# Kernel tuning notes

Hardware: AMD Instinct MI355X
Metric: run time of the kernel (lower is better)

## Reference

```python
import jax, jax.numpy as jnp
import numpy as np

L = 2      # layer_num
H = 64     # hid_dim == in_dim (required by final .view(B, N, F))


def setup_inputs() -> dict:
    key = jax.random.key(0)
    k = jax.random.split(key, 5)
    B, T, N, Fd = 64, 48, 256, H
    s = 1.0 / np.sqrt(H)  # PyTorch GRUCell init scale
    return {
        "x": jax.random.normal(k[0], (B, T, N, Fd), dtype=jnp.float32),
        "Wih": jax.random.uniform(k[1], (L, 3 * H, H), minval=-s, maxval=s, dtype=jnp.float32),
        "Whh": jax.random.uniform(k[2], (L, 3 * H, H), minval=-s, maxval=s, dtype=jnp.float32),
        "bih": jax.random.uniform(k[3], (L, 3 * H), minval=-s, maxval=s, dtype=jnp.float32),
        "bhh": jax.random.uniform(k[4], (L, 3 * H), minval=-s, maxval=s, dtype=jnp.float32),
    }


def _ngru_forward(x, Wih, Whh, bih, bhh):
    B, T, N, Fd = x.shape
    # (T, B*N, F): time-major sequence; each layer sees the SAME input x_t
    # (layers are parallel, not stacked, per the original module).
    xs = x.transpose(1, 0, 2, 3).reshape(T, B * N, Fd)
    h0 = jnp.zeros((L, B * N, H), dtype=x.dtype)

    def step(h, x_t):
        # gi: (L, B*N, 3H), gh: (L, B*N, 3H)
        gi = jnp.einsum('bf,lgf->lbg', x_t, Wih) + bih[:, None, :]
        gh = jnp.einsum('lbh,lgh->lbg', h, Whh) + bhh[:, None, :]
        gi_r, gi_z, gi_n = jnp.split(gi, 3, axis=-1)
        gh_r, gh_z, gh_n = jnp.split(gh, 3, axis=-1)
        r = jax.nn.sigmoid(gi_r + gh_r)
        z = jax.nn.sigmoid(gi_z + gh_z)
        n = jnp.tanh(gi_n + r * gh_n)
        h_new = (1.0 - z) * n + z * h
        return h_new, None

    h_final, _ = jax.lax.scan(step, h0, xs)
    # out = h of LAST layer, viewed back as (B, N, F) (requires H == Fd)
    return h_final[-1].reshape(B, N, H)


def reference(x, Wih, Whh, bih, bhh):
    return _ngru_forward(x, Wih, Whh, bih, bhh)
```

## Files before the change

### kernel.cpp

```cpp
#include <hip/hip_runtime.h>
#include <math.h>


#define TT 48
#define HH 64
#define GG 192
#define NN 256
#define RPB 32
#define NTHREADS 512
#define AK 136
#define HBUF (RPB*AK)

typedef _Float16 h8 __attribute__((ext_vector_type(8)));
typedef __attribute__((ext_vector_type(4))) float f32x4;
typedef __attribute__((ext_vector_type(2))) unsigned u32x2;

__device__ __forceinline__ float sigm(float v) {
    return __builtin_amdgcn_rcpf(1.f + __expf(-v));
}
__device__ __forceinline__ float tanh_f(float v) {
    float a = fabsf(v);
    float e = __expf(2.f * a);
    float t = 1.f - 2.f * __builtin_amdgcn_rcpf(e + 1.f);
    return v < 0.f ? -t : t;
}
__device__ __forceinline__ unsigned pkh2(float a, float b) {
    union { _Float16 h[2]; unsigned u; } c;
    c.h[0] = (_Float16)a; c.h[1] = (_Float16)b;
    return c.u;
}

#define MF(A, B, C) __builtin_amdgcn_mfma_f32_16x16x32_f16(A, B, C, 0, 0, 0)

__global__ __launch_bounds__(NTHREADS)
__attribute__((amdgpu_waves_per_eu(4, 4)))
void ngru_mfma12(const float* __restrict__ x,
                 const float* __restrict__ Wih,
                 const float* __restrict__ Whh,
                 const float* __restrict__ bih,
                 const float* __restrict__ bhh,
                 float* __restrict__ out)
{
    extern __shared__ __align__(16) _Float16 lds_h[];

    const int tid  = threadIdx.x;
    const int lane = tid & 63;
    const int wv   = tid >> 6;
    const int m    = wv >> 2;
    const int nw   = wv & 3;
    const int c0   = lane & 15;
    const int rq   = lane >> 4;
    const int j    = nw * 16 + c0;

    const int grow0 = blockIdx.x * RPB;
    const int bb    = grow0 / NN;
    const int n0    = grow0 % NN;

    const float* Wi = Wih + GG * HH;
    const float* Wh = Whh + GG * HH;

    h8 Bf[12];
    #pragma unroll
    for (int g = 0; g < 4; ++g) {
        const int ktlo = (g == 3) ? 2 : 0;
        const int kthi = (g == 2) ? 2 : 4;
        #pragma unroll
        for (int kt = ktlo; kt < kthi; ++kt) {
            const int slot = (g < 2) ? g * 4 + kt : 8 + (g - 2) * 2 + (kt & 1);
            const bool isWi = (kt < 2);
            const int gbase = (g >= 2) ? 2 : g;
            const float* src = (isWi ? Wi : Wh)
                             + (gbase * 64 + j) * HH + (kt & 1) * 32 + rq * 8;
            h8 f;
            #pragma unroll
            for (int q = 0; q < 8; ++q) f[q] = (_Float16)src[q];
            Bf[slot] = f;
        }
    }

    const float brz  = bih[GG + j]      + bhh[GG + j];
    const float bzz  = bih[GG + 64 + j] + bhh[GG + 64 + j];
    const float bin_ = bih[GG + 128 + j];
    const float bhn_ = bhh[GG + 128 + j];

    const int xrow = tid >> 4;
    const int xc   = (tid & 15) * 4;
    {
        *(u32x2*)(lds_h + xrow * AK + 64 + xc) = (u32x2){0u, 0u};
        const float* xsrc = x + ((size_t)(bb * TT) * NN + n0 + xrow) * HH + xc;
        float4 p = *(const float4*)xsrc;
        *(u32x2*)(lds_h + xrow * AK + xc) = (u32x2){pkh2(p.x, p.y), pkh2(p.z, p.w)};
    }

    float hreg[4];
    #pragma unroll
    for (int r = 0; r < 4; ++r) hreg[r] = 0.f;

    __syncthreads();

    for (int t = 0; t < TT; ++t) {
        _Float16* cur = lds_h + (t & 1) * HBUF;
        _Float16* nxt = lds_h + ((t & 1) ^ 1) * HBUF;
        const bool hasNext = (t + 1 < TT);

        float4 p;
        if (hasNext)
            p = *(const float4*)(x + ((size_t)(bb * TT + t + 1) * NN
                                      + n0 + xrow) * HH + xc);

        f32x4 acc0 = {brz,  brz,  brz,  brz };
        f32x4 acc1 = {bzz,  bzz,  bzz,  bzz };
        f32x4 acc2 = {bin_, bin_, bin_, bin_};
        f32x4 acc3 = {bhn_, bhn_, bhn_, bhn_};

        const _Float16* ab = cur + (m * 16 + c0) * AK + rq * 8;
        h8 A0 = *(const h8*)(ab);
        h8 A1 = *(const h8*)(ab + 32);
        h8 A2 = *(const h8*)(ab + 64);
        h8 A3 = *(const h8*)(ab + 96);

        __builtin_amdgcn_s_setprio(1);
        acc0 = MF(A0, Bf[0], acc0);
        acc0 = MF(A1, Bf[1], acc0);
        acc0 = MF(A2, Bf[2], acc0);
        acc0 = MF(A3, Bf[3], acc0);
        acc1 = MF(A0, Bf[4], acc1);
        acc1 = MF(A1, Bf[5], acc1);
        acc1 = MF(A2, Bf[6], acc1);
        acc1 = MF(A3, Bf[7], acc1);
        acc2 = MF(A0, Bf[8], acc2);
        acc2 = MF(A1, Bf[9], acc2);
        acc3 = MF(A2, Bf[10], acc3);
        acc3 = MF(A3, Bf[11], acc3);
        __builtin_amdgcn_s_setprio(0);

        #pragma unroll
        for (int r = 0; r < 4; ++r) {
            const int row = m * 16 + rq * 4 + r;
            float rg = sigm(acc0[r]);
            float zg = sigm(acc1[r]);
            float ng = tanh_f(fmaf(rg, acc3[r], acc2[r]));
            float hn = fmaf(zg, hreg[r] - ng, ng);
            hreg[r] = hn;
            if (hasNext)
                nxt[row * AK + 64 + j] = (_Float16)hn;
        }

        if (hasNext) {
            *(u32x2*)(nxt + xrow * AK + xc) =
                (u32x2){pkh2(p.x, p.y), pkh2(p.z, p.w)};
            __syncthreads();
        }
    }

    #pragma unroll
    for (int r = 0; r < 4; ++r)
        out[(size_t)(grow0 + m * 16 + rq * 4 + r) * HH + j] = hreg[r];
}

extern "C" void kernel_launch(void* const* d_in, const int* in_sizes, int n_in,
                              void* d_out, int out_size, void* d_ws, size_t ws_size,
                              hipStream_t stream) {
    const float* x   = (const float*)d_in[0];
    const float* Wih = (const float*)d_in[1];
    const float* Whh = (const float*)d_in[2];
    const float* bih = (const float*)d_in[3];
    const float* bhh = (const float*)d_in[4];
    float* out = (float*)d_out;

    const int lds_bytes = 2 * HBUF * (int)sizeof(_Float16);
    (void)hipFuncSetAttribute((const void*)ngru_mfma12,
                        hipFuncAttributeMaxDynamicSharedMemorySize, lds_bytes);

    dim3 grid(16384 / RPB);
    dim3 block(NTHREADS);
    ngru_mfma12<<<grid, block, lds_bytes, stream>>>(x, Wih, Whh, bih, bhh, out);
}
```

Measured before the change: 68.75 us.

## Ping-pong two row groups so MFMA of one overlaps epilogue of other

Each block now handles 64 rows split into two 32-row wave groups that alternate phases. While one group runs the MFMA gate matmuls for its rows, the other runs the sigmoid/tanh epilogue and stages the next x tile. The goal is to hide the serial matmul-then-elementwise dependency on the MFMA and VALU units. Each wave now owns two 16-row tiles, and waves-per-EU is lowered to 2. That halves the grid and adds a second barrier per timestep, at the cost of occupancy and extra register pressure.

New measurement: 79.77 us. 1.16x slower.

```diff
diff --git a/kernel.cpp b/kernel.cpp
--- a/kernel.cpp
+++ b/kernel.cpp
@@ -6,14 +6,14 @@
 #define HH 64
 #define GG 192
 #define NN 256
-#define RPB 32
+#define RPB 64
 #define NTHREADS 512
 #define AK 136
 #define HBUF (RPB*AK)
 
 typedef _Float16 h8 __attribute__((ext_vector_type(8)));
 typedef __attribute__((ext_vector_type(4))) float f32x4;
-typedef __attribute__((ext_vector_type(2))) unsigned u32x2;
+typedef __attribute__((ext_vector_type(4))) unsigned u32x4;
 
 __device__ __forceinline__ float sigm(float v) {
     return __builtin_amdgcn_rcpf(1.f + __expf(-v));
@@ -33,8 +33,8 @@
 #define MF(A, B, C) __builtin_amdgcn_mfma_f32_16x16x32_f16(A, B, C, 0, 0, 0)
 
 __global__ __launch_bounds__(NTHREADS)
-__attribute__((amdgpu_waves_per_eu(4, 4)))
-void ngru_mfma12(const float* __restrict__ x,
+__attribute__((amdgpu_waves_per_eu(2, 2)))
+void ngru_mfma13(const float* __restrict__ x,
                  const float* __restrict__ Wih,
                  const float* __restrict__ Whh,
                  const float* __restrict__ bih,
@@ -46,11 +46,12 @@
     const int tid  = threadIdx.x;
     const int lane = tid & 63;
     const int wv   = tid >> 6;
-    const int m    = wv >> 2;
+    const int grp  = wv >> 2;
     const int nw   = wv & 3;
     const int c0   = lane & 15;
     const int rq   = lane >> 4;
     const int j    = nw * 16 + c0;
+    const int rbase = grp * 32;
 
     const int grow0 = blockIdx.x * RPB;
     const int bb    = grow0 / NN;
@@ -83,79 +84,131 @@
     const float bin_ = bih[GG + 128 + j];
     const float bhn_ = bhh[GG + 128 + j];
 
-    const int xrow = tid >> 4;
-    const int xc   = (tid & 15) * 4;
     {
-        *(u32x2*)(lds_h + xrow * AK + 64 + xc) = (u32x2){0u, 0u};
-        const float* xsrc = x + ((size_t)(bb * TT) * NN + n0 + xrow) * HH + xc;
-        float4 p = *(const float4*)xsrc;
-        *(u32x2*)(lds_h + xrow * AK + xc) = (u32x2){pkh2(p.x, p.y), pkh2(p.z, p.w)};
-    }
-
-    float hreg[4];
+        const int zr = tid >> 3;
+        const int zc = (tid & 7) * 8;
+        *(u32x4*)(lds_h + zr * AK + 64 + zc) = (u32x4){0u, 0u, 0u, 0u};
+        const float* xsrc = x + ((size_t)(bb * TT) * NN + n0 + zr) * HH + zc;
+        float4 a = *(const float4*)xsrc;
+        float4 b = *(const float4*)(xsrc + 4);
+        *(u32x4*)(lds_h + zr * AK + zc) =
+            (u32x4){pkh2(a.x, a.y), pkh2(a.z, a.w), pkh2(b.x, b.y), pkh2(b.z, b.w)};
+    }
+
+    const int gt   = tid & 255;
+    const int srow = rbase + (gt >> 3);
+    const int skc  = (gt & 7) * 8;
+
+    float hreg[2][4];
     #pragma unroll
-    for (int r = 0; r < 4; ++r) hreg[r] = 0.f;
+    for (int m = 0; m < 2; ++m)
+        #pragma unroll
+        for (int r = 0; r < 4; ++r) hreg[m][r] = 0.f;
+
+    f32x4 a00, a01, a02, a03, a10, a11, a12, a13;
+    float4 pa, pb;
+
+#define MFMA_BLOCK(BUF)                                                        \
+    {                                                                          \
+        const _Float16* ab0 = (BUF) + (rbase + c0) * AK + rq * 8;              \
+        const _Float16* ab1 = ab0 + 16 * AK;                                   \
+        h8 A0 = *(const h8*)(ab0);                                             \
+        h8 A1 = *(const h8*)(ab0 + 32);                                        \
+        h8 A2 = *(const h8*)(ab0 + 64);                                        \
+        h8 A3 = *(const h8*)(ab0 + 96);                                        \
+        h8 C0 = *(const h8*)(ab1);                                             \
+        h8 C1 = *(const h8*)(ab1 + 32);                                        \
+        h8 C2 = *(const h8*)(ab1 + 64);                                        \
+        h8 C3 = *(const h8*)(ab1 + 96);                                        \
+        a00 = (f32x4){brz,  brz,  brz,  brz };                                 \
+        a01 = (f32x4){bzz,  bzz,  bzz,  bzz };                                 \
+        a02 = (f32x4){bin_, bin_, bin_, bin_};                                 \
+        a03 = (f32x4){bhn_, bhn_, bhn_, bhn_};                                 \
+        a10 = a00; a11 = a01; a12 = a02; a13 = a03;                            \
+        __builtin_amdgcn_s_setprio(1);                                         \
+        a00 = MF(A0, Bf[0], a00);  a00 = MF(A1, Bf[1], a00);                   \
+        a00 = MF(A2, Bf[2], a00);  a00 = MF(A3, Bf[3], a00);                   \
+        a01 = MF(A0, Bf[4], a01);  a01 = MF(A1, Bf[5], a01);                   \
+        a01 = MF(A2, Bf[6], a01);  a01 = MF(A3, Bf[7], a01);                   \
+        a02 = MF(A0, Bf[8], a02);  a02 = MF(A1, Bf[9], a02);                   \
+        a03 = MF(A2, Bf[10], a03); a03 = MF(A3, Bf[11], a03);                  \
+        a10 = MF(C0, Bf[0], a10);  a10 = MF(C1, Bf[1], a10);                   \
+        a10 = MF(C2, Bf[2], a10);  a10 = MF(C3, Bf[3], a10);                   \
+        a11 = MF(C0, Bf[4], a11);  a11 = MF(C1, Bf[5], a11);                   \
+        a11 = MF(C2, Bf[6], a11);  a11 = MF(C3, Bf[7], a11);                   \
+        a12 = MF(C0, Bf[8], a12);  a12 = MF(C1, Bf[9], a12);                   \
+        a13 = MF(C2, Bf[10], a13); a13 = MF(C3, Bf[11], a13);                  \
+        __builtin_amdgcn_s_setprio(0);                                         \
+    }
+
+#define EPI_M(AM0, AM1, AM2, AM3, M, NXT, WR)                                  \
+    _Pragma("unroll") for (int r = 0; r < 4; ++r) {                            \
+        const int row = rbase + (M) * 16 + rq * 4 + r;                         \
+        float rg = sigm(AM0[r]);                                               \
+        float zg = sigm(AM1[r]);                                               \
+        float ng = tanh_f(fmaf(rg, AM3[r], AM2[r]));                           \
+        float hn = fmaf(zg, hreg[M][r] - ng, ng);                              \
+        hreg[M][r] = hn;                                                       \
+        if (WR) (NXT)[row * AK + 64 + j] = (_Float16)hn;                       \
+    }
+
+#define LOAD_X(T1)                                                             \
+    {                                                                          \
+        const float* xs =                                                      \
+            x + ((size_t)(bb * TT + (T1)) * NN + n0 + srow) * HH + skc;        \
+        pa = *(const float4*)xs;                                               \
+        pb = *(const float4*)(xs + 4);                                         \
+    }
+
+#define STAGE_X(NXT)                                                           \
+    *(u32x4*)((NXT) + srow * AK + skc) =                                       \
+        (u32x4){pkh2(pa.x, pa.y), pkh2(pa.z, pa.w),                            \
+                pkh2(pb.x, pb.y), pkh2(pb.z, pb.w)};
 
     __syncthreads();
+
+    if (grp) {
+        if (TT > 1) LOAD_X(1);
+        MFMA_BLOCK(lds_h);
+    }
 
     for (int t = 0; t < TT; ++t) {
         _Float16* cur = lds_h + (t & 1) * HBUF;
         _Float16* nxt = lds_h + ((t & 1) ^ 1) * HBUF;
         const bool hasNext = (t + 1 < TT);
 
-        float4 p;
-        if (hasNext)
-            p = *(const float4*)(x + ((size_t)(bb * TT + t + 1) * NN
-                                      + n0 + xrow) * HH + xc);
-
-        f32x4 acc0 = {brz,  brz,  brz,  brz };
-        f32x4 acc1 = {bzz,  bzz,  bzz,  bzz };
-        f32x4 acc2 = {bin_, bin_, bin_, bin_};
-        f32x4 acc3 = {bhn_, bhn_, bhn_, bhn_};
-
-        const _Float16* ab = cur + (m * 16 + c0) * AK + rq * 8;
-        h8 A0 = *(const h8*)(ab);
-        h8 A1 = *(const h8*)(ab + 32);
-        h8 A2 = *(const h8*)(ab + 64);
-        h8 A3 = *(const h8*)(ab + 96);
-
-        __builtin_amdgcn_s_setprio(1);
-        acc0 = MF(A0, Bf[0], acc0);
-        acc0 = MF(A1, Bf[1], acc0);
-        acc0 = MF(A2, Bf[2], acc0);
-        acc0 = MF(A3, Bf[3], acc0);
-        acc1 = MF(A0, Bf[4], acc1);
-        acc1 = MF(A1, Bf[5], acc1);
-        acc1 = MF(A2, Bf[6], acc1);
-        acc1 = MF(A3, Bf[7], acc1);
-        acc2 = MF(A0, Bf[8], acc2);
-        acc2 = MF(A1, Bf[9], acc2);
-        acc3 = MF(A2, Bf[10], acc3);
-        acc3 = MF(A3, Bf[11], acc3);
-        __builtin_amdgcn_s_setprio(0);
-
+        if (!grp) {
+            if (hasNext) LOAD_X(t + 1);
+            MFMA_BLOCK(cur);
+        } else {
+            EPI_M(a00, a01, a02, a03, 0, nxt, hasNext);
+            EPI_M(a10, a11, a12, a13, 1, nxt, hasNext);
+            if (hasNext) STAGE_X(nxt);
+        }
+        __syncthreads();
+
+        if (!grp) {
+            EPI_M(a00, a01, a02, a03, 0, nxt, hasNext);
+            EPI_M(a10, a11, a12, a13, 1, nxt, hasNext);
+            if (hasNext) STAGE_X(nxt);
+        } else if (hasNext) {
+            if (t + 2 < TT) LOAD_X(t + 2);
+            MFMA_BLOCK(nxt);
+        }
+        __syncthreads();
+    }
+
+#undef MFMA_BLOCK
+#undef EPI_M
+#undef LOAD_X
+#undef STAGE_X
+
+    #pragma unroll
+    for (int m = 0; m < 2; ++m)
         #pragma unroll
-        for (int r = 0; r < 4; ++r) {
-            const int row = m * 16 + rq * 4 + r;
-            float rg = sigm(acc0[r]);
-            float zg = sigm(acc1[r]);
-            float ng = tanh_f(fmaf(rg, acc3[r], acc2[r]));
-            float hn = fmaf(zg, hreg[r] - ng, ng);
-            hreg[r] = hn;
-            if (hasNext)
-                nxt[row * AK + 64 + j] = (_Float16)hn;
-        }
-
-        if (hasNext) {
-            *(u32x2*)(nxt + xrow * AK + xc) =
-                (u32x2){pkh2(p.x, p.y), pkh2(p.z, p.w)};
-            __syncthreads();
-        }
-    }
-
-    #pragma unroll
-    for (int r = 0; r < 4; ++r)
-        out[(size_t)(grow0 + m * 16 + rq * 4 + r) * HH + j] = hreg[r];
+        for (int r = 0; r < 4; ++r)
+            out[(size_t)(grow0 + rbase + m * 16 + rq * 4 + r) * HH + j] =
+                hreg[m][r];
 }
 
 extern "C" void kernel_launch(void* const* d_in, const int* in_sizes, int n_in,
@@ -169,10 +222,10 @@
     float* out = (float*)d_out;
 
     const int lds_bytes = 2 * HBUF * (int)sizeof(_Float16);
-    (void)hipFuncSetAttribute((const void*)ngru_mfma12,
+    (void)hipFuncSetAttribute((const void*)ngru_mfma13,
                         hipFuncAttributeMaxDynamicSharedMemorySize, lds_bytes);
 
     dim3 grid(16384 / RPB);
     dim3 block(NTHREADS);
-    ngru_mfma12<<<grid, block, lds_bytes, stream>>>(x, Wih, Whh, bih, bhh, out);
-}
+    ngru_mfma13<<<grid, block, lds_bytes, stream>>>(x, Wih, Whh, bih, bhh, out);
+}
```

## Give each wave all 64 hidden columns to eliminate block barriers

Applied to the files above, without the earlier changes.

Restructures the GRU kernel so each wave owns 16 rows and computes all 64 hidden columns, keeping all weight fragments in registers with one wave per EU. Each wave uses a private LDS buffer, so the per-timestep __syncthreads across 8 waves is removed. The trade-off is far fewer waves per SIMD and a longer serial MFMA/transcendental chain per step, reducing latency hiding and raising register pressure.

After: 103.0 us. +49.8%, slower.

```diff
diff --git a/kernel.cpp b/kernel.cpp
--- a/kernel.cpp
+++ b/kernel.cpp
@@ -6,14 +6,14 @@
 #define HH 64
 #define GG 192
 #define NN 256
-#define RPB 32
-#define NTHREADS 512
+#define RPW 16
+#define NTHREADS 256
 #define AK 136
-#define HBUF (RPB*AK)
+#define WBUF (RPW*AK)
 
 typedef _Float16 h8 __attribute__((ext_vector_type(8)));
 typedef __attribute__((ext_vector_type(4))) float f32x4;
-typedef __attribute__((ext_vector_type(2))) unsigned u32x2;
+typedef __attribute__((ext_vector_type(4))) unsigned u32x4;
 
 __device__ __forceinline__ float sigm(float v) {
     return __builtin_amdgcn_rcpf(1.f + __expf(-v));
@@ -33,8 +33,8 @@
 #define MF(A, B, C) __builtin_amdgcn_mfma_f32_16x16x32_f16(A, B, C, 0, 0, 0)
 
 __global__ __launch_bounds__(NTHREADS)
-__attribute__((amdgpu_waves_per_eu(4, 4)))
-void ngru_mfma12(const float* __restrict__ x,
+__attribute__((amdgpu_waves_per_eu(1, 1)))
+void ngru_mfma16(const float* __restrict__ x,
                  const float* __restrict__ Wih,
                  const float* __restrict__ Whh,
                  const float* __restrict__ bih,
@@ -46,116 +46,139 @@
     const int tid  = threadIdx.x;
     const int lane = tid & 63;
     const int wv   = tid >> 6;
-    const int m    = wv >> 2;
-    const int nw   = wv & 3;
     const int c0   = lane & 15;
     const int rq   = lane >> 4;
-    const int j    = nw * 16 + c0;
-
-    const int grow0 = blockIdx.x * RPB;
+    _Float16* buf  = lds_h + wv * WBUF;
+
+    const int grow0 = blockIdx.x * 64 + wv * RPW;
     const int bb    = grow0 / NN;
     const int n0    = grow0 % NN;
 
     const float* Wi = Wih + GG * HH;
     const float* Wh = Whh + GG * HH;
 
-    h8 Bf[12];
-    #pragma unroll
-    for (int g = 0; g < 4; ++g) {
-        const int ktlo = (g == 3) ? 2 : 0;
-        const int kthi = (g == 2) ? 2 : 4;
-        #pragma unroll
-        for (int kt = ktlo; kt < kthi; ++kt) {
-            const int slot = (g < 2) ? g * 4 + kt : 8 + (g - 2) * 2 + (kt & 1);
-            const bool isWi = (kt < 2);
-            const int gbase = (g >= 2) ? 2 : g;
-            const float* src = (isWi ? Wi : Wh)
-                             + (gbase * 64 + j) * HH + (kt & 1) * 32 + rq * 8;
-            h8 f;
+    h8 Bx[3][4][2], Bh[3][4][2];
+    #pragma unroll
+    for (int g = 0; g < 3; ++g)
+        #pragma unroll
+        for (int jt = 0; jt < 4; ++jt)
             #pragma unroll
-            for (int q = 0; q < 8; ++q) f[q] = (_Float16)src[q];
-            Bf[slot] = f;
+            for (int kt = 0; kt < 2; ++kt) {
+                const int jrow = g * 64 + jt * 16 + c0;
+                const float* si = Wi + jrow * HH + kt * 32 + rq * 8;
+                const float* sh = Wh + jrow * HH + kt * 32 + rq * 8;
+                h8 fi, fh;
+                #pragma unroll
+                for (int q = 0; q < 8; ++q) {
+                    fi[q] = (_Float16)si[q];
+                    fh[q] = (_Float16)sh[q];
+                }
+                Bx[g][jt][kt] = fi;
+                Bh[g][jt][kt] = fh;
+            }
+
+    float brz[4], bzz[4], bin_[4], bhn_[4];
+    #pragma unroll
+    for (int jt = 0; jt < 4; ++jt) {
+        const int jj = jt * 16 + c0;
+        brz[jt]  = bih[GG + jj]       + bhh[GG + jj];
+        bzz[jt]  = bih[GG + 64 + jj]  + bhh[GG + 64 + jj];
+        bin_[jt] = bih[GG + 128 + jj];
+        bhn_[jt] = bhh[GG + 128 + jj];
+    }
+
+    const int srow = lane >> 2;
+    const int scol = (lane & 3) * 16;
+
+    {
+        u32x4 z = {0u, 0u, 0u, 0u};
+        *(u32x4*)(buf + srow * AK + 64 + scol)     = z;
+        *(u32x4*)(buf + srow * AK + 64 + scol + 8) = z;
+
+        const float* xs = x + ((size_t)(bb * TT) * NN + n0 + srow) * HH + scol;
+        float4 q0 = *(const float4*)xs;
+        float4 q1 = *(const float4*)(xs + 4);
+        float4 q2 = *(const float4*)(xs + 8);
+        float4 q3 = *(const float4*)(xs + 12);
+        u32x4 w0 = {pkh2(q0.x,q0.y), pkh2(q0.z,q0.w),
+                    pkh2(q1.x,q1.y), pkh2(q1.z,q1.w)};
+        u32x4 w1 = {pkh2(q2.x,q2.y), pkh2(q2.z,q2.w),
+                    pkh2(q3.x,q3.y), pkh2(q3.z,q3.w)};
+        *(u32x4*)(buf + srow * AK + scol)     = w0;
+        *(u32x4*)(buf + srow * AK + scol + 8) = w1;
+    }
+
+    float hreg[4][4];
+    #pragma unroll
+    for (int jt = 0; jt < 4; ++jt)
+        #pragma unroll
+        for (int r = 0; r < 4; ++r) hreg[jt][r] = 0.f;
+
+    const f32x4 Z4 = {0.f, 0.f, 0.f, 0.f};
+
+    #pragma unroll 1
+    for (int t = 0; t < TT; ++t) {
+        h8 A0 = *(const h8*)(buf + c0 * AK + 0  + rq * 8);
+        h8 A1 = *(const h8*)(buf + c0 * AK + 32 + rq * 8);
+        h8 A2 = *(const h8*)(buf + c0 * AK + 64 + rq * 8);
+        h8 A3 = *(const h8*)(buf + c0 * AK + 96 + rq * 8);
+
+        const int tn = (t + 1 < TT) ? t + 1 : t;
+        const float* xs =
+            x + ((size_t)(bb * TT + tn) * NN + n0 + srow) * HH + scol;
+        float4 q0 = *(const float4*)xs;
+        float4 q1 = *(const float4*)(xs + 4);
+        float4 q2 = *(const float4*)(xs + 8);
+        float4 q3 = *(const float4*)(xs + 12);
+
+        f32x4 ar[4], az[4], ai[4], ah[4];
+        #pragma unroll
+        for (int jt = 0; jt < 4; ++jt) {
+            ar[jt] = MF(A0, Bx[0][jt][0], Z4);
+            ar[jt] = MF(A1, Bx[0][jt][1], ar[jt]);
+            ar[jt] = MF(A2, Bh[0][jt][0], ar[jt]);
+            ar[jt] = MF(A3, Bh[0][jt][1], ar[jt]);
+            az[jt] = MF(A0, Bx[1][jt][0], Z4);
+            az[jt] = MF(A1, Bx[1][jt][1], az[jt]);
+            az[jt] = MF(A2, Bh[1][jt][0], az[jt]);
+            az[jt] = MF(A3, Bh[1][jt][1], az[jt]);
+            ai[jt] = MF(A0, Bx[2][jt][0], Z4);
+            ai[jt] = MF(A1, Bx[2][jt][1], ai[jt]);
+            ah[jt] = MF(A2, Bh[2][jt][0], Z4);
+            ah[jt] = MF(A3, Bh[2][jt][1], ah[jt]);
         }
+
+        #pragma unroll
+        for (int jt = 0; jt < 4; ++jt) {
+            #pragma unroll
+            for (int r = 0; r < 4; ++r) {
+                float sr  = ar[jt][r] + brz[jt];
+                float sz  = az[jt][r] + bzz[jt];
+                float gin = ai[jt][r] + bin_[jt];
+                float ghn = ah[jt][r] + bhn_[jt];
+                float rg = sigm(sr);
+                float zg = sigm(sz);
+                float ng = tanh_f(fmaf(rg, ghn, gin));
+                float hn = fmaf(zg, hreg[jt][r] - ng, ng);
+                hreg[jt][r] = hn;
+                buf[(rq * 4 + r) * AK + 64 + jt * 16 + c0] = (_Float16)hn;
+            }
+        }
+
+        u32x4 w0 = {pkh2(q0.x,q0.y), pkh2(q0.z,q0.w),
+                    pkh2(q1.x,q1.y), pkh2(q1.z,q1.w)};
+        u32x4 w1 = {pkh2(q2.x,q2.y), pkh2(q2.z,q2.w),
+                    pkh2(q3.x,q3.y), pkh2(q3.z,q3.w)};
+        *(u32x4*)(buf + srow * AK + scol)     = w0;
+        *(u32x4*)(buf + srow * AK + scol + 8) = w1;
     }
 
-    const float brz  = bih[GG + j]      + bhh[GG + j];
-    const float bzz  = bih[GG + 64 + j] + bhh[GG + 64 + j];
-    const float bin_ = bih[GG + 128 + j];
-    const float bhn_ = bhh[GG + 128 + j];
-
-    const int xrow = tid >> 4;
-    const int xc   = (tid & 15) * 4;
-    {
-        *(u32x2*)(lds_h + xrow * AK + 64 + xc) = (u32x2){0u, 0u};
-        const float* xsrc = x + ((size_t)(bb * TT) * NN + n0 + xrow) * HH + xc;
-        float4 p = *(const float4*)xsrc;
-        *(u32x2*)(lds_h + xrow * AK + xc) = (u32x2){pkh2(p.x, p.y), pkh2(p.z, p.w)};
-    }
-
-    float hreg[4];
-    #pragma unroll
-    for (int r = 0; r < 4; ++r) hreg[r] = 0.f;
-
-    __syncthreads();
-
-    for (int t = 0; t < TT; ++t) {
-        _Float16* cur = lds_h + (t & 1) * HBUF;
-        _Float16* nxt = lds_h + ((t & 1) ^ 1) * HBUF;
-        const bool hasNext = (t + 1 < TT);
-
-        float4 p;
-        if (hasNext)
-            p = *(const float4*)(x + ((size_t)(bb * TT + t + 1) * NN
-                                      + n0 + xrow) * HH + xc);
-
-        f32x4 acc0 = {brz,  brz,  brz,  brz };
-        f32x4 acc1 = {bzz,  bzz,  bzz,  bzz };
-        f32x4 acc2 = {bin_, bin_, bin_, bin_};
-        f32x4 acc3 = {bhn_, bhn_, bhn_, bhn_};
-
-        const _Float16* ab = cur + (m * 16 + c0) * AK + rq * 8;
-        h8 A0 = *(const h8*)(ab);
-        h8 A1 = *(const h8*)(ab + 32);
-        h8 A2 = *(const h8*)(ab + 64);
-        h8 A3 = *(const h8*)(ab + 96);
-
-        __builtin_amdgcn_s_setprio(1);
-        acc0 = MF(A0, Bf[0], acc0);
-        acc0 = MF(A1, Bf[1], acc0);
-        acc0 = MF(A2, Bf[2], acc0);
-        acc0 = MF(A3, Bf[3], acc0);
-        acc1 = MF(A0, Bf[4], acc1);
-        acc1 = MF(A1, Bf[5], acc1);
-        acc1 = MF(A2, Bf[6], acc1);
-        acc1 = MF(A3, Bf[7], acc1);
-        acc2 = MF(A0, Bf[8], acc2);
-        acc2 = MF(A1, Bf[9], acc2);
-        acc3 = MF(A2, Bf[10], acc3);
-        acc3 = MF(A3, Bf[11], acc3);
-        __builtin_amdgcn_s_setprio(0);
-
-        #pragma unroll
-        for (int r = 0; r < 4; ++r) {
-            const int row = m * 16 + rq * 4 + r;
-            float rg = sigm(acc0[r]);
-            float zg = sigm(acc1[r]);
-            float ng = tanh_f(fmaf(rg, acc3[r], acc2[r]));
-            float hn = fmaf(zg, hreg[r] - ng, ng);
-            hreg[r] = hn;
-            if (hasNext)
-                nxt[row * AK + 64 + j] = (_Float16)hn;
-        }
-
-        if (hasNext) {
-            *(u32x2*)(nxt + xrow * AK + xc) =
-                (u32x2){pkh2(p.x, p.y), pkh2(p.z, p.w)};
-            __syncthreads();
-        }
-    }
-
-    #pragma unroll
-    for (int r = 0; r < 4; ++r)
-        out[(size_t)(grow0 + m * 16 + rq * 4 + r) * HH + j] = hreg[r];
+    #pragma unroll
+    for (int jt = 0; jt < 4; ++jt)
+        #pragma unroll
+        for (int r = 0; r < 4; ++r)
+            out[(size_t)(grow0 + rq * 4 + r) * HH + jt * 16 + c0] =
+                hreg[jt][r];
 }
 
 extern "C" void kernel_launch(void* const* d_in, const int* in_sizes, int n_in,
@@ -168,11 +191,11 @@
     const float* bhh = (const float*)d_in[4];
     float* out = (float*)d_out;
 
-    const int lds_bytes = 2 * HBUF * (int)sizeof(_Float16);
-    (void)hipFuncSetAttribute((const void*)ngru_mfma12,
+    const int lds_bytes = 4 * WBUF * (int)sizeof(_Float16);
+    (void)hipFuncSetAttribute((const void*)ngru_mfma16,
                         hipFuncAttributeMaxDynamicSharedMemorySize, lds_bytes);
 
-    dim3 grid(16384 / RPB);
+    dim3 grid(16384 / 64);
     dim3 block(NTHREADS);
-    ngru_mfma12<<<grid, block, lds_bytes, stream>>>(x, Wih, Whh, bih, bhh, out);
-}
+    ngru_mfma16<<<grid, block, lds_bytes, stream>>>(x, Wih, Whh, bih, bhh, out);
+}
```
